# Kernel tuning notes

Measured on AMD Instinct MI355X. Metric: run time of the kernel, lower is better.

The kernel has to match this reference:

```python
import jax, jax.numpy as jnp
import numpy as np

EPS = 1e-12  # matches torch F.normalize default eps


def _l2_normalize(x, axis):
    n = jnp.sqrt(jnp.sum(x * x, axis=axis, keepdims=True))
    return x / jnp.maximum(n, EPS)


def _sp_loss(x, r, weight):
    # x, r: [B, C, M, N]; weight: [C]
    B, C, M, N = x.shape
    # trace(matmul(norm_rows(x), norm_rows(r).T)) == sum over rows of cosine sim
    xr = _l2_normalize(x, axis=3)
    rr = _l2_normalize(r, axis=3)
    a_per = jnp.sum(xr * rr, axis=(2, 3)) / M  # [B, C]
    xc = _l2_normalize(x, axis=2)
    rc = _l2_normalize(r, axis=2)
    b_per = jnp.sum(xc * rc, axis=(2, 3)) / N  # [B, C]
    a = jnp.sum(a_per * weight[None, :])
    b = jnp.sum(b_per * weight[None, :])
    return (-a / B) + (-b / B)


def _image_gradients(x):
    # x: [B, C, H, W]
    f_v = x[:, :, :, :-1] - x[:, :, :, 1:]  # [B, C, H, W-1]
    f_h = x[:, :, :-1, :] - x[:, :, 1:, :]  # [B, C, H-1, W]
    return f_v, f_h


def setup_inputs() -> dict:
    key = jax.random.key(0)
    k1, k2 = jax.random.split(key)
    B, C, H, W = 32, 3, 512, 512
    inp = jax.random.normal(k1, (B, C, H, W), dtype=jnp.float32)
    ref = jax.random.normal(k2, (B, C, H, W), dtype=jnp.float32)
    return {"input": inp, "reference": ref}


def reference(input, reference):
    weight = jnp.array([1.0, 1.0, 1.0], dtype=input.dtype)
    iv, ih = _image_gradients(input)
    rv, rh = _image_gradients(reference)
    return _sp_loss(iv, rv, weight) + _sp_loss(ih, rh, weight)
```

## Files before the change

kernel.cpp:

```cpp
#include <hip/hip_runtime.h>


#define DPP_ADD(x, ctrl, rmask) \
  x += __int_as_float(__builtin_amdgcn_update_dpp(0, __float_as_int(x), ctrl, rmask, 0xf, false))

__device__ __forceinline__ float wave_dpp_sum(float x){
  DPP_ADD(x, 0x111, 0xf);
  DPP_ADD(x, 0x112, 0xf);
  DPP_ADD(x, 0x114, 0xf);
  DPP_ADD(x, 0x118, 0xf);
  DPP_ADD(x, 0x142, 0xa);
  DPP_ADD(x, 0x143, 0xc);
  return x;
}

__device__ __forceinline__ float cos_sim(float d, float sx, float sr){
  float nx = fmaxf(sqrtf(sx), 1e-12f);
  float nr = fmaxf(sqrtf(sr), 1e-12f);
  return d / (nx * nr);
}

__global__ __launch_bounds__(256) void gp_uni(
    const float* __restrict__ X, const float* __restrict__ R,
    float* __restrict__ rowPart, float* __restrict__ colPart)
{
  const int bid = blockIdx.x;
  const int p = bid >> 4, q = bid & 15;
  const int tid = threadIdx.x, w = tid >> 6, l = tid & 63;
  const int half = w >> 1;
  const int wp   = w & 1;
  const size_t plane = (size_t)p * (512u*512u);
  const float* xp = X + plane;
  const float* rp = R + plane;
  const int c  = wp*256 + 4*l;
  const int cn = (c+4 < 512) ? c+4 : 511;
  const bool tlast = (c == 508);
  const int h0 = q*32 + half*16;

  __shared__ float colbuf[6][512];
  __shared__ float rowbuf[32][2][6];

  float cv0[4], cv1[4], cv2[4], ch0[4], ch1[4], ch2[4];
  #pragma unroll
  for (int j = 0; j < 4; ++j){
    cv0[j]=0.f; cv1[j]=0.f; cv2[j]=0.f;
    ch0[j]=0.f; ch1[j]=0.f; ch2[j]=0.f;
  }

  const float* xr0 = xp + (size_t)h0*512;
  const float* rr0 = rp + (size_t)h0*512;
  float4 xc4 = *(const float4*)(xr0 + c);
  float4 rc4 = *(const float4*)(rr0 + c);
  float  xhv = xr0[cn], rhv = rr0[cn];

  #pragma unroll 2
  for (int k = 0; k < 16; ++k){
    const int h  = h0 + k;
    const int hn = (h+1 < 512) ? h+1 : 511;
    const float* xr = xp + (size_t)hn*512;
    const float* rr = rp + (size_t)hn*512;
    const float4 nx4 = *(const float4*)(xr + c);
    const float4 nr4 = *(const float4*)(rr + c);
    const float  nxh = xr[cn], nrh = rr[cn];

    const float ax[4] = {xc4.x, xc4.y, xc4.z, xc4.w};
    const float ar[4] = {rc4.x, rc4.y, rc4.z, rc4.w};
    const float bx[4] = {nx4.x, nx4.y, nx4.z, nx4.w};
    const float br[4] = {nr4.x, nr4.y, nr4.z, nr4.w};

    float dv[4], ev[4];
    dv[0]=ax[0]-ax[1]; dv[1]=ax[1]-ax[2]; dv[2]=ax[2]-ax[3];
    ev[0]=ar[0]-ar[1]; ev[1]=ar[1]-ar[2]; ev[2]=ar[2]-ar[3];
    dv[3] = tlast ? 0.f : (ax[3]-xhv);
    ev[3] = tlast ? 0.f : (ar[3]-rhv);

    float p0=0.f,p1=0.f,p2=0.f, q0=0.f,q1=0.f,q2=0.f;
    #pragma unroll
    for (int j = 0; j < 4; ++j){
      p0 = fmaf(dv[j],ev[j],p0); p1 = fmaf(dv[j],dv[j],p1); p2 = fmaf(ev[j],ev[j],p2);
      cv0[j] = fmaf(dv[j],ev[j],cv0[j]);
      cv1[j] = fmaf(dv[j],dv[j],cv1[j]);
      cv2[j] = fmaf(ev[j],ev[j],cv2[j]);
      const float dh = ax[j]-bx[j];
      const float eh = ar[j]-br[j];
      q0 = fmaf(dh,eh,q0); q1 = fmaf(dh,dh,q1); q2 = fmaf(eh,eh,q2);
      ch0[j] = fmaf(dh,eh,ch0[j]);
      ch1[j] = fmaf(dh,dh,ch1[j]);
      ch2[j] = fmaf(eh,eh,ch2[j]);
    }

    p0 = wave_dpp_sum(p0); p1 = wave_dpp_sum(p1); p2 = wave_dpp_sum(p2);
    q0 = wave_dpp_sum(q0); q1 = wave_dpp_sum(q1); q2 = wave_dpp_sum(q2);
    if (l == 63){
      const int rr_ = half*16 + k;
      rowbuf[rr_][wp][0]=p0; rowbuf[rr_][wp][1]=p1; rowbuf[rr_][wp][2]=p2;
      rowbuf[rr_][wp][3]=q0; rowbuf[rr_][wp][4]=q1; rowbuf[rr_][wp][5]=q2;
    }

    xc4 = nx4; rc4 = nr4; xhv = nxh; rhv = nrh;
  }

  if (half == 0){
    *(float4*)&colbuf[0][c] = make_float4(cv0[0],cv0[1],cv0[2],cv0[3]);
    *(float4*)&colbuf[1][c] = make_float4(cv1[0],cv1[1],cv1[2],cv1[3]);
    *(float4*)&colbuf[2][c] = make_float4(cv2[0],cv2[1],cv2[2],cv2[3]);
    *(float4*)&colbuf[3][c] = make_float4(ch0[0],ch0[1],ch0[2],ch0[3]);
    *(float4*)&colbuf[4][c] = make_float4(ch1[0],ch1[1],ch1[2],ch1[3]);
    *(float4*)&colbuf[5][c] = make_float4(ch2[0],ch2[1],ch2[2],ch2[3]);
  }
  __syncthreads();
  if (half == 1){
    float4 t;
    t = *(float4*)&colbuf[0][c]; t.x+=cv0[0]; t.y+=cv0[1]; t.z+=cv0[2]; t.w+=cv0[3]; *(float4*)&colbuf[0][c]=t;
    t = *(float4*)&colbuf[1][c]; t.x+=cv1[0]; t.y+=cv1[1]; t.z+=cv1[2]; t.w+=cv1[3]; *(float4*)&colbuf[1][c]=t;
    t = *(float4*)&colbuf[2][c]; t.x+=cv2[0]; t.y+=cv2[1]; t.z+=cv2[2]; t.w+=cv2[3]; *(float4*)&colbuf[2][c]=t;
    t = *(float4*)&colbuf[3][c]; t.x+=ch0[0]; t.y+=ch0[1]; t.z+=ch0[2]; t.w+=ch0[3]; *(float4*)&colbuf[3][c]=t;
    t = *(float4*)&colbuf[4][c]; t.x+=ch1[0]; t.y+=ch1[1]; t.z+=ch1[2]; t.w+=ch1[3]; *(float4*)&colbuf[4][c]=t;
    t = *(float4*)&colbuf[5][c]; t.x+=ch2[0]; t.y+=ch2[1]; t.z+=ch2[2]; t.w+=ch2[3]; *(float4*)&colbuf[5][c]=t;
  }
  __syncthreads();
  float4* slot = (float4*)(colPart + (size_t)bid * (6*512));
  const float4* cb = (const float4*)colbuf;
  #pragma unroll
  for (int i = 0; i < 3; ++i) slot[tid + 256*i] = cb[tid + 256*i];

  if (tid < 64){
    float rv = 0.f, rh = 0.f;
    if (tid < 32){
      const float a0 = rowbuf[tid][0][0] + rowbuf[tid][1][0];
      const float a1 = rowbuf[tid][0][1] + rowbuf[tid][1][1];
      const float a2 = rowbuf[tid][0][2] + rowbuf[tid][1][2];
      const float b0 = rowbuf[tid][0][3] + rowbuf[tid][1][3];
      const float b1 = rowbuf[tid][0][4] + rowbuf[tid][1][4];
      const float b2 = rowbuf[tid][0][5] + rowbuf[tid][1][5];
      rv = cos_sim(a0,a1,a2);
      const int h = q*32 + tid;
      rh = (h < 511) ? cos_sim(b0,b1,b2) : 0.f;
    }
    rv = wave_dpp_sum(rv);
    rh = wave_dpp_sum(rh);
    if (tid == 63){
      rowPart[2*bid+0] = rv;
      rowPart[2*bid+1] = rh;
    }
  }
}

__global__ __launch_bounds__(256) void gp_cols(
    const float* __restrict__ colPart, double* __restrict__ dblk)
{
  const int p = blockIdx.x >> 1;
  const int f = blockIdx.x & 1;
  const int tid = threadIdx.x;
  double acc = 0.0;
  for (int c = tid; c < 512; c += 256){
    float d = 0.f, a = 0.f, b = 0.f;
    #pragma unroll
    for (int s = 0; s < 16; ++s){
      const float* sp = colPart + ((size_t)(p*16 + s) * 6 + f*3) * 512;
      d += sp[c]; a += sp[512 + c]; b += sp[1024 + c];
    }
    acc += (double)cos_sim(d, a, b);
  }
  #pragma unroll
  for (int m = 1; m < 64; m <<= 1) acc += __shfl_xor(acc, m, 64);
  __shared__ double ls[4];
  const int w = tid >> 6, l = tid & 63;
  if (l == 0) ls[w] = acc;
  __syncthreads();
  if (tid == 0) dblk[blockIdx.x] = ls[0] + ls[1] + ls[2] + ls[3];
}

__global__ __launch_bounds__(256) void gp_fin(
    const double* __restrict__ dblk, const float* __restrict__ rowPart,
    int nblk, float* __restrict__ out)
{
  const int tid = threadIdx.x;
  double rv = 0, rh = 0, cv = 0, ch = 0;
  for (int i = tid; i < nblk; i += 256){
    rv += (double)rowPart[2*i];
    rh += (double)rowPart[2*i+1];
  }
  for (int i = tid; i < 192; i += 256){
    if (i & 1) ch += dblk[i]; else cv += dblk[i];
  }
  #pragma unroll
  for (int m = 1; m < 64; m <<= 1){
    rv += __shfl_xor(rv, m, 64); rh += __shfl_xor(rh, m, 64);
    cv += __shfl_xor(cv, m, 64); ch += __shfl_xor(ch, m, 64);
  }
  __shared__ double ls[4][4];
  const int w = tid >> 6, l = tid & 63;
  if (l == 0){ ls[w][0]=rv; ls[w][1]=rh; ls[w][2]=cv; ls[w][3]=ch; }
  __syncthreads();
  if (tid == 0){
    double RV=0, RH=0, CV=0, CH=0;
    #pragma unroll
    for (int i = 0; i < 4; ++i){ RV+=ls[i][0]; RH+=ls[i][1]; CV+=ls[i][2]; CH+=ls[i][3]; }
    const double t = RV/512.0 + RH/511.0 + CV/511.0 + CH/512.0;
    out[0] = (float)(-t / 32.0);
  }
}

extern "C" void kernel_launch(void* const* d_in, const int* in_sizes, int n_in,
                              void* d_out, int out_size, void* d_ws, size_t ws_size,
                              hipStream_t stream) {
  const float* X = (const float*)d_in[0];
  const float* R = (const float*)d_in[1];
  float* out = (float*)d_out;

  float*  colPart = (float*)d_ws;
  float*  rowPart = colPart + (size_t)96*16*6*512;
  double* dblk    = (double*)(rowPart + (size_t)1536*2);

  gp_uni <<<dim3(1536), dim3(256), 0, stream>>>(X, R, rowPart, colPart);
  gp_cols<<<dim3(192),  dim3(256), 0, stream>>>(colPart, dblk);
  gp_fin <<<dim3(1),    dim3(256), 0, stream>>>(dblk, rowPart, 1536, out);
}
```

Baseline: 51.87 us.

## Give each wave a full 512-wide row and fold row cosines in-wave

Each wave now covers an entire 512-column row with 8 columns per lane and processes 8 rows, instead of two waves splitting each row across 16 rows. The right-neighbour halo comes from a lane shuffle rather than an extra scalar global load. Row cosine similarities are computed and accumulated per wave, which removes the rowbuf shared array and its cross-wave reduction. Column partials are combined through two shared buffers. The cost is more live registers per thread (48 accumulators) under a launch bound of 4 blocks, and four times as many row partials going to the final kernel.

```diff
diff --git a/kernel.cpp b/kernel.cpp
--- a/kernel.cpp
+++ b/kernel.cpp
@@ -1,5 +1,7 @@
 #include <hip/hip_runtime.h>
 
+
+typedef float f32x4 __attribute__((ext_vector_type(4)));
 
 #define DPP_ADD(x, ctrl, rmask) \
   x += __int_as_float(__builtin_amdgcn_update_dpp(0, __float_as_int(x), ctrl, rmask, 0xf, false))
@@ -20,67 +22,62 @@
   return d / (nx * nr);
 }
 
-__global__ __launch_bounds__(256) void gp_uni(
+__global__ __launch_bounds__(256, 4) void gp_uni(
     const float* __restrict__ X, const float* __restrict__ R,
     float* __restrict__ rowPart, float* __restrict__ colPart)
 {
   const int bid = blockIdx.x;
   const int p = bid >> 4, q = bid & 15;
   const int tid = threadIdx.x, w = tid >> 6, l = tid & 63;
-  const int half = w >> 1;
-  const int wp   = w & 1;
-  const size_t plane = (size_t)p * (512u*512u);
+  const size_t plane = (size_t)p * (512u * 512u);
   const float* xp = X + plane;
   const float* rp = R + plane;
-  const int c  = wp*256 + 4*l;
-  const int cn = (c+4 < 512) ? c+4 : 511;
-  const bool tlast = (c == 508);
-  const int h0 = q*32 + half*16;
-
-  __shared__ float colbuf[6][512];
-  __shared__ float rowbuf[32][2][6];
-
-  float cv0[4], cv1[4], cv2[4], ch0[4], ch1[4], ch2[4];
+  const int c = 8 * l;
+  const bool tlast = (l == 63);
+  const int h0 = q*32 + w*8;
+
+  __shared__ float Abuf[6][512];
+  __shared__ float Bbuf[6][512];
+
+  float cv0[8], cv1[8], cv2[8], ch0[8], ch1[8], ch2[8];
   #pragma unroll
-  for (int j = 0; j < 4; ++j){
+  for (int j = 0; j < 8; ++j){
     cv0[j]=0.f; cv1[j]=0.f; cv2[j]=0.f;
     ch0[j]=0.f; ch1[j]=0.f; ch2[j]=0.f;
   }
-
-  const float* xr0 = xp + (size_t)h0*512;
-  const float* rr0 = rp + (size_t)h0*512;
-  float4 xc4 = *(const float4*)(xr0 + c);
-  float4 rc4 = *(const float4*)(rr0 + c);
-  float  xhv = xr0[cn], rhv = rr0[cn];
+  float rsv = 0.f, rsh = 0.f;
+
+  const float* xr = xp + (size_t)h0*512 + c;
+  const float* rr = rp + (size_t)h0*512 + c;
+  float4 xa = *(const float4*)xr, xb = *(const float4*)(xr+4);
+  float4 ra = *(const float4*)rr, rb = *(const float4*)(rr+4);
 
   #pragma unroll 2
-  for (int k = 0; k < 16; ++k){
+  for (int k = 0; k < 8; ++k){
     const int h  = h0 + k;
     const int hn = (h+1 < 512) ? h+1 : 511;
-    const float* xr = xp + (size_t)hn*512;
-    const float* rr = rp + (size_t)hn*512;
-    const float4 nx4 = *(const float4*)(xr + c);
-    const float4 nr4 = *(const float4*)(rr + c);
-    const float  nxh = xr[cn], nrh = rr[cn];
-
-    const float ax[4] = {xc4.x, xc4.y, xc4.z, xc4.w};
-    const float ar[4] = {rc4.x, rc4.y, rc4.z, rc4.w};
-    const float bx[4] = {nx4.x, nx4.y, nx4.z, nx4.w};
-    const float br[4] = {nr4.x, nr4.y, nr4.z, nr4.w};
-
-    float dv[4], ev[4];
-    dv[0]=ax[0]-ax[1]; dv[1]=ax[1]-ax[2]; dv[2]=ax[2]-ax[3];
-    ev[0]=ar[0]-ar[1]; ev[1]=ar[1]-ar[2]; ev[2]=ar[2]-ar[3];
-    dv[3] = tlast ? 0.f : (ax[3]-xhv);
-    ev[3] = tlast ? 0.f : (ar[3]-rhv);
+    const float* xn = xp + (size_t)hn*512 + c;
+    const float* rn = rp + (size_t)hn*512 + c;
+    const float4 nxa = *(const float4*)xn, nxb = *(const float4*)(xn+4);
+    const float4 nra = *(const float4*)rn, nrb = *(const float4*)(rn+4);
+
+    const float xhalo = __shfl_down(xa.x, 1, 64);
+    const float rhalo = __shfl_down(ra.x, 1, 64);
+
+    const float ax[8] = {xa.x,xa.y,xa.z,xa.w, xb.x,xb.y,xb.z,xb.w};
+    const float ar[8] = {ra.x,ra.y,ra.z,ra.w, rb.x,rb.y,rb.z,rb.w};
+    const float bx[8] = {nxa.x,nxa.y,nxa.z,nxa.w, nxb.x,nxb.y,nxb.z,nxb.w};
+    const float br[8] = {nra.x,nra.y,nra.z,nra.w, nrb.x,nrb.y,nrb.z,nrb.w};
 
     float p0=0.f,p1=0.f,p2=0.f, q0=0.f,q1=0.f,q2=0.f;
     #pragma unroll
-    for (int j = 0; j < 4; ++j){
-      p0 = fmaf(dv[j],ev[j],p0); p1 = fmaf(dv[j],dv[j],p1); p2 = fmaf(ev[j],ev[j],p2);
-      cv0[j] = fmaf(dv[j],ev[j],cv0[j]);
-      cv1[j] = fmaf(dv[j],dv[j],cv1[j]);
-      cv2[j] = fmaf(ev[j],ev[j],cv2[j]);
+    for (int j = 0; j < 8; ++j){
+      const float dv = (j<7) ? (ax[j]-ax[j+1]) : (tlast ? 0.f : (ax[7]-xhalo));
+      const float ev = (j<7) ? (ar[j]-ar[j+1]) : (tlast ? 0.f : (ar[7]-rhalo));
+      p0 = fmaf(dv,ev,p0); p1 = fmaf(dv,dv,p1); p2 = fmaf(ev,ev,p2);
+      cv0[j] = fmaf(dv,ev,cv0[j]);
+      cv1[j] = fmaf(dv,dv,cv1[j]);
+      cv2[j] = fmaf(ev,ev,cv2[j]);
       const float dh = ax[j]-bx[j];
       const float eh = ar[j]-br[j];
       q0 = fmaf(dh,eh,q0); q1 = fmaf(dh,dh,q1); q2 = fmaf(eh,eh,q2);
@@ -91,58 +88,52 @@
 
     p0 = wave_dpp_sum(p0); p1 = wave_dpp_sum(p1); p2 = wave_dpp_sum(p2);
     q0 = wave_dpp_sum(q0); q1 = wave_dpp_sum(q1); q2 = wave_dpp_sum(q2);
-    if (l == 63){
-      const int rr_ = half*16 + k;
-      rowbuf[rr_][wp][0]=p0; rowbuf[rr_][wp][1]=p1; rowbuf[rr_][wp][2]=p2;
-      rowbuf[rr_][wp][3]=q0; rowbuf[rr_][wp][4]=q1; rowbuf[rr_][wp][5]=q2;
-    }
-
-    xc4 = nx4; rc4 = nr4; xhv = nxh; rhv = nrh;
-  }
-
-  if (half == 0){
-    *(float4*)&colbuf[0][c] = make_float4(cv0[0],cv0[1],cv0[2],cv0[3]);
-    *(float4*)&colbuf[1][c] = make_float4(cv1[0],cv1[1],cv1[2],cv1[3]);
-    *(float4*)&colbuf[2][c] = make_float4(cv2[0],cv2[1],cv2[2],cv2[3]);
-    *(float4*)&colbuf[3][c] = make_float4(ch0[0],ch0[1],ch0[2],ch0[3]);
-    *(float4*)&colbuf[4][c] = make_float4(ch1[0],ch1[1],ch1[2],ch1[3]);
-    *(float4*)&colbuf[5][c] = make_float4(ch2[0],ch2[1],ch2[2],ch2[3]);
-  }
-  __syncthreads();
-  if (half == 1){
-    float4 t;
-    t = *(float4*)&colbuf[0][c]; t.x+=cv0[0]; t.y+=cv0[1]; t.z+=cv0[2]; t.w+=cv0[3]; *(float4*)&colbuf[0][c]=t;
-    t = *(float4*)&colbuf[1][c]; t.x+=cv1[0]; t.y+=cv1[1]; t.z+=cv1[2]; t.w+=cv1[3]; *(float4*)&colbuf[1][c]=t;
-    t = *(float4*)&colbuf[2][c]; t.x+=cv2[0]; t.y+=cv2[1]; t.z+=cv2[2]; t.w+=cv2[3]; *(float4*)&colbuf[2][c]=t;
-    t = *(float4*)&colbuf[3][c]; t.x+=ch0[0]; t.y+=ch0[1]; t.z+=ch0[2]; t.w+=ch0[3]; *(float4*)&colbuf[3][c]=t;
-    t = *(float4*)&colbuf[4][c]; t.x+=ch1[0]; t.y+=ch1[1]; t.z+=ch1[2]; t.w+=ch1[3]; *(float4*)&colbuf[4][c]=t;
-    t = *(float4*)&colbuf[5][c]; t.x+=ch2[0]; t.y+=ch2[1]; t.z+=ch2[2]; t.w+=ch2[3]; *(float4*)&colbuf[5][c]=t;
-  }
-  __syncthreads();
-  float4* slot = (float4*)(colPart + (size_t)bid * (6*512));
-  const float4* cb = (const float4*)colbuf;
-  #pragma unroll
-  for (int i = 0; i < 3; ++i) slot[tid + 256*i] = cb[tid + 256*i];
-
-  if (tid < 64){
-    float rv = 0.f, rh = 0.f;
-    if (tid < 32){
-      const float a0 = rowbuf[tid][0][0] + rowbuf[tid][1][0];
-      const float a1 = rowbuf[tid][0][1] + rowbuf[tid][1][1];
-      const float a2 = rowbuf[tid][0][2] + rowbuf[tid][1][2];
-      const float b0 = rowbuf[tid][0][3] + rowbuf[tid][1][3];
-      const float b1 = rowbuf[tid][0][4] + rowbuf[tid][1][4];
-      const float b2 = rowbuf[tid][0][5] + rowbuf[tid][1][5];
-      rv = cos_sim(a0,a1,a2);
-      const int h = q*32 + tid;
-      rh = (h < 511) ? cos_sim(b0,b1,b2) : 0.f;
-    }
-    rv = wave_dpp_sum(rv);
-    rh = wave_dpp_sum(rh);
-    if (tid == 63){
-      rowPart[2*bid+0] = rv;
-      rowPart[2*bid+1] = rh;
-    }
+    rsv += cos_sim(p0,p1,p2);
+    if (h < 511) rsh += cos_sim(q0,q1,q2);
+
+    xa = nxa; xb = nxb; ra = nra; rb = nrb;
+  }
+
+  if (w == 0){
+    #pragma unroll
+    for (int j = 0; j < 8; ++j){
+      Abuf[0][c+j]=cv0[j]; Abuf[1][c+j]=cv1[j]; Abuf[2][c+j]=cv2[j];
+      Abuf[3][c+j]=ch0[j]; Abuf[4][c+j]=ch1[j]; Abuf[5][c+j]=ch2[j];
+    }
+  } else if (w == 2){
+    #pragma unroll
+    for (int j = 0; j < 8; ++j){
+      Bbuf[0][c+j]=cv0[j]; Bbuf[1][c+j]=cv1[j]; Bbuf[2][c+j]=cv2[j];
+      Bbuf[3][c+j]=ch0[j]; Bbuf[4][c+j]=ch1[j]; Bbuf[5][c+j]=ch2[j];
+    }
+  }
+  __syncthreads();
+  if (w == 1){
+    #pragma unroll
+    for (int j = 0; j < 8; ++j){
+      Abuf[0][c+j]+=cv0[j]; Abuf[1][c+j]+=cv1[j]; Abuf[2][c+j]+=cv2[j];
+      Abuf[3][c+j]+=ch0[j]; Abuf[4][c+j]+=ch1[j]; Abuf[5][c+j]+=ch2[j];
+    }
+  } else if (w == 3){
+    #pragma unroll
+    for (int j = 0; j < 8; ++j){
+      Bbuf[0][c+j]+=cv0[j]; Bbuf[1][c+j]+=cv1[j]; Bbuf[2][c+j]+=cv2[j];
+      Bbuf[3][c+j]+=ch0[j]; Bbuf[4][c+j]+=ch1[j]; Bbuf[5][c+j]+=ch2[j];
+    }
+  }
+  __syncthreads();
+  {
+    const f32x4* A4 = (const f32x4*)Abuf;
+    const f32x4* B4 = (const f32x4*)Bbuf;
+    f32x4* s4 = (f32x4*)(colPart + (size_t)bid * (6*512));
+    #pragma unroll
+    for (int i = 0; i < 3; ++i)
+      s4[tid + 256*i] = A4[tid + 256*i] + B4[tid + 256*i];
+  }
+
+  if (l == 63){
+    rowPart[(bid*4 + w)*2 + 0] = rsv;
+    rowPart[(bid*4 + w)*2 + 1] = rsh;
   }
 }
 
@@ -211,9 +202,9 @@
 
   float*  colPart = (float*)d_ws;
   float*  rowPart = colPart + (size_t)96*16*6*512;
-  double* dblk    = (double*)(rowPart + (size_t)1536*2);
+  double* dblk    = (double*)(rowPart + (size_t)6144*2);
 
   gp_uni <<<dim3(1536), dim3(256), 0, stream>>>(X, R, rowPart, colPart);
   gp_cols<<<dim3(192),  dim3(256), 0, stream>>>(colPart, dblk);
-  gp_fin <<<dim3(1),    dim3(256), 0, stream>>>(dblk, rowPart, 1536, out);
-}
+  gp_fin <<<dim3(1),    dim3(256), 0, stream>>>(dblk, rowPart, 6144, out);
+}
```

Result: slower. 123.5 us (+138.0%).
